# Performance work log

Hardware: AMD Instinct MI355X
Metric: run time of the kernel (lower is better)

The kernel has to match this reference:

```python
import jax, jax.numpy as jnp
import numpy as np

Nc, Nd, Ns = 8000, 6000, 6000          # circRNA / drug / disease node counts
F, H, O = 64, 4, 64                    # feature dim (fcir=fdrug=fdis), GAT heads, cnn out_channels
Ec, Ed, Es = 256000, 192000, 192000    # directed edge counts per graph
NEG_SLOPE = 0.2


def _gcn(x, src, dst, ew, W, b, N):
    # PyG GCNConv w/ edge_weight: add self loops (w=1), symmetric norm, x@W.T, scatter-add
    loop = jnp.arange(N, dtype=src.dtype)
    s = jnp.concatenate([src, loop])
    d = jnp.concatenate([dst, loop])
    w = jnp.concatenate([ew, jnp.ones((N,), x.dtype)])
    deg = jax.ops.segment_sum(w, d, num_segments=N)
    dinv = jnp.where(deg > 0, jax.lax.rsqrt(deg), 0.0)
    norm = dinv[s] * w * dinv[d]                        # [E+N]
    h = x @ W.T                                         # [N,F]
    return jax.ops.segment_sum(h[s] * norm[:, None], d, num_segments=N) + b


def _gat(x, src, dst, ew, W, a_src, a_dst, We, a_edge, b, N):
    # PyG GATConv(heads=H, concat=False, edge_dim=1); self loops with fill_value='mean'
    E = src.shape[0]
    ea = ew[:, None]                                    # [E,1]
    cnt = jax.ops.segment_sum(jnp.ones((E,), x.dtype), dst, num_segments=N)
    esum = jax.ops.segment_sum(ea, dst, num_segments=N)
    loop_attr = esum / jnp.maximum(cnt, 1.0)[:, None]   # per-dst mean edge attr
    loop = jnp.arange(N, dtype=src.dtype)
    s = jnp.concatenate([src, loop])
    d = jnp.concatenate([dst, loop])
    ea = jnp.concatenate([ea, loop_attr], axis=0)       # [E+N,1]
    h = (x @ W.T).reshape(N, H, F)
    al_s = jnp.einsum('nhf,hf->nh', h, a_src)
    al_d = jnp.einsum('nhf,hf->nh', h, a_dst)
    e = (ea @ We.T).reshape(-1, H, F)
    al_e = jnp.einsum('ehf,hf->eh', e, a_edge)
    alpha = al_s[s] + al_d[d] + al_e                    # [E+N,H]
    alpha = jnp.where(alpha >= 0, alpha, NEG_SLOPE * alpha)   # leaky_relu
    amax = jax.ops.segment_max(alpha, d, num_segments=N)
    ex = jnp.exp(alpha - amax[d])
    denom = jax.ops.segment_sum(ex, d, num_segments=N)
    coef = ex / denom[d]                                # segment softmax over incoming edges
    out = jax.ops.segment_sum(h[s] * coef[:, :, None], d, num_segments=N)  # [N,H,F]
    return out.mean(axis=1) + b                         # concat=False -> head mean


def _readout(x1, x2, W, b):
    # Conv1d(in=2, out=O, kernel=(F,1)) on [1,2,F,N] == full contraction over (layer, feature)
    X = jnp.stack([x1, x2], axis=0)                     # [2,N,F]
    return jnp.einsum('cnf,ocf->no', X, W) + b          # [N,O]


def _forward(fl, cir_edges, drug_edges, dis_edges):
    def branch(x, ei, ew, g1W, g1b, gaW, gas, gad, gaeW, gae, gab, g2W, g2b, N):
        src, dst = ei[0], ei[1]
        f1 = jax.nn.relu(_gcn(x, src, dst, ew, g1W, g1b, N))
        att = jax.nn.relu(_gat(f1, src, dst, ew, gaW, gas, gad, gaeW, gae, gab, N))
        f2 = jax.nn.relu(_gcn(att, src, dst, ew, g2W, g2b, N))
        return f1, f2

    cf1, cf2 = branch(fl['x_cir'], cir_edges, fl['cir_ew'], fl['gcn_cir1_W'], fl['gcn_cir1_b'],
                      fl['gat_cir_W'], fl['gat_cir_asrc'], fl['gat_cir_adst'], fl['gat_cir_eW'],
                      fl['gat_cir_aedge'], fl['gat_cir_b'], fl['gcn_cir2_W'], fl['gcn_cir2_b'], Nc)
    # NOTE: the source forward reuses the *_dis GCN/GAT layers for the drug branch (faithful)
    df1, df2 = branch(fl['x_drug'], drug_edges, fl['drug_ew'], fl['gcn_dis1_W'], fl['gcn_dis1_b'],
                      fl['gat_dis_W'], fl['gat_dis_asrc'], fl['gat_dis_adst'], fl['gat_dis_eW'],
                      fl['gat_dis_aedge'], fl['gat_dis_b'], fl['gcn_dis2_W'], fl['gcn_dis2_b'], Nd)
    sf1, sf2 = branch(fl['x_dis'], dis_edges, fl['dis_ew'], fl['gcn_dis1_W'], fl['gcn_dis1_b'],
                      fl['gat_dis_W'], fl['gat_dis_asrc'], fl['gat_dis_adst'], fl['gat_dis_eW'],
                      fl['gat_dis_aedge'], fl['gat_dis_b'], fl['gcn_dis2_W'], fl['gcn_dis2_b'], Ns)
    cir_fea = _readout(cf1, cf2, fl['cnn_cir_W'], fl['cnn_cir_b'])
    drug_fea = _readout(df1, df2, fl['cnn_dis_W'], fl['cnn_dis_b'])   # source uses cnn_dis for drug too
    dis_fea = _readout(sf1, sf2, fl['cnn_dis_W'], fl['cnn_dis_b'])
    return (cir_fea @ dis_fea.T, cir_fea @ drug_fea.T, drug_fea @ dis_fea.T,
            cir_fea, drug_fea, dis_fea)


_PARAM_SHAPES = [
    ('gcn_cir1_W', (F, F)), ('gcn_cir1_b', (F,)),
    ('gcn_cir2_W', (F, F)), ('gcn_cir2_b', (F,)),
    ('gcn_dis1_W', (F, F)), ('gcn_dis1_b', (F,)),
    ('gcn_dis2_W', (F, F)), ('gcn_dis2_b', (F,)),
    ('gat_cir_W', (H * F, F)), ('gat_cir_asrc', (H, F)), ('gat_cir_adst', (H, F)),
    ('gat_cir_eW', (H * F, 1)), ('gat_cir_aedge', (H, F)), ('gat_cir_b', (F,)),
    ('gat_dis_W', (H * F, F)), ('gat_dis_asrc', (H, F)), ('gat_dis_adst', (H, F)),
    ('gat_dis_eW', (H * F, 1)), ('gat_dis_aedge', (H, F)), ('gat_dis_b', (F,)),
    ('cnn_cir_W', (O, 2, F)), ('cnn_cir_b', (O,)),
    ('cnn_dis_W', (O, 2, F)), ('cnn_dis_b', (O,)),
]


def setup_inputs() -> dict:
    key = jax.random.key(0)
    ks = iter(jax.random.split(key, 64))
    inp = {}
    inp['x_cir'] = jax.random.normal(next(ks), (Nc, F), jnp.float32)
    inp['x_drug'] = jax.random.normal(next(ks), (Nd, F), jnp.float32)
    inp['x_dis'] = jax.random.normal(next(ks), (Ns, F), jnp.float32)
    inp['cir_edges'] = jax.random.randint(next(ks), (2, Ec), 0, Nc, dtype=jnp.int32)
    inp['cir_ew'] = jax.random.uniform(next(ks), (Ec,), jnp.float32)
    inp['drug_edges'] = jax.random.randint(next(ks), (2, Ed), 0, Nd, dtype=jnp.int32)
    inp['drug_ew'] = jax.random.uniform(next(ks), (Ed,), jnp.float32)
    inp['dis_edges'] = jax.random.randint(next(ks), (2, Es), 0, Ns, dtype=jnp.int32)
    inp['dis_ew'] = jax.random.uniform(next(ks), (Es,), jnp.float32)
    for name, shape in _PARAM_SHAPES:
        inp[name] = jax.random.normal(next(ks), shape, jnp.float32) * 0.1
    return inp


def reference(x_cir, x_drug, x_dis, cir_edges, cir_ew, drug_edges, drug_ew, dis_edges, dis_ew,
              gcn_cir1_W, gcn_cir1_b, gcn_cir2_W, gcn_cir2_b,
              gcn_dis1_W, gcn_dis1_b, gcn_dis2_W, gcn_dis2_b,
              gat_cir_W, gat_cir_asrc, gat_cir_adst, gat_cir_eW, gat_cir_aedge, gat_cir_b,
              gat_dis_W, gat_dis_asrc, gat_dis_adst, gat_dis_eW, gat_dis_aedge, gat_dis_b,
              cnn_cir_W, cnn_cir_b, cnn_dis_W, cnn_dis_b):
    fl = {k: v for k, v in locals().items() if k not in ('cir_edges', 'drug_edges', 'dis_edges')}
    return _forward(fl, cir_edges, drug_edges, dis_edges)
```

## Files before the change

kernel.cpp:

```cpp
#include <hip/hip_runtime.h>

#define NEG_SLOPE 0.2f

typedef __attribute__((ext_vector_type(8))) short bfrag;
typedef __attribute__((ext_vector_type(4))) float f32x4;

static __device__ __forceinline__ ushort f2bf(float x){
  uint u = __float_as_uint(x);
  uint r = (u + 0x7fff + ((u>>16)&1)) >> 16;
  return (ushort)r;
}
static __device__ __forceinline__ float bf2f(ushort h){
  return __uint_as_float(((uint)h)<<16);
}


struct G3 {
  const int* src[3]; const int* dst[3]; const float* ew[3];
  float* deg[3]; int* cnt[3]; int* pos[3];
  float* dinv[3]; float* lat[3]; int* rowp[3];
  int* esrc[3]; float* eww[3];
  int N[3]; int E[3];
};

struct MM3 {
  const float* A[3]; const float* B[3]; float* C[3]; const float* bias[3];
  ushort* H[3]; ushort* L[3];
  const float* gas[3]; const float* gad[3];
  float* als[3]; float* ald[3];
  int M[3]; int lda, ldb, N2;
};

struct AGG3 {
  const float* h[3]; const float* dinv[3]; const int* rowp[3];
  const int* esrc[3]; const float* eww[3]; const float* bias[3];
  float* out[3]; int N[3]; int ostride, ooff;
};

struct GAT3 {
  const float* hg[3]; const float* als[3]; const float* ald[3];
  const float* lat[3]; const float* ce[3]; const int* rowp[3];
  const int* esrc[3]; const float* eww[3]; const float* bias[3];
  float* out[3]; int N[3];
};

struct SC3 {
  const ushort* AH[3]; const ushort* AL[3];
  const ushort* BH[3]; const ushort* BL[3];
  float* C[3]; int M[3]; int N2;
};


__global__ void k_init_b(G3 g){
  int b = blockIdx.z;
  int i = blockIdx.x*blockDim.x + threadIdx.x;
  if (i < g.N[b]){ g.deg[b][i] = 1.0f; g.cnt[b][i] = 0; g.pos[b][i] = 0; }
}

__global__ void k_edge_stats_b(G3 g){
  int b = blockIdx.z;
  int e = blockIdx.x*blockDim.x + threadIdx.x;
  if (e < g.E[b]){
    int d = g.dst[b][e];
    atomicAdd(&g.deg[b][d], g.ew[b][e]);
    atomicAdd(&g.cnt[b][d], 1);
  }
}

__global__ void k_scan_b(G3 g, const float* gaeW_c, const float* gae_c, float* ce_c,
                         const float* gaeW_d, const float* gae_d, float* ce_d){
  int b = blockIdx.x;
  int tid = threadIdx.x;
  if (b < 2 && tid < 64){
    const float* W = b ? gaeW_d : gaeW_c;
    const float* Aa = b ? gae_d : gae_c;
    float* ceo = b ? ce_d : ce_c;
    #pragma unroll
    for (int hh=0; hh<4; hh++){
      float v = W[hh*64+tid] * Aa[hh*64+tid];
      #pragma unroll
      for (int off=32; off>0; off>>=1) v += __shfl_down(v,off);
      if (tid==0) ceo[hh] = v;
    }
  }
  int N = g.N[b];
  const float* deg = g.deg[b];
  const int* cnt = g.cnt[b];
  float* dinv = g.dinv[b];
  float* lat = g.lat[b];
  int* rowp = g.rowp[b];
  const int T = 1024, PER = 8;
  __shared__ int ssum[T];
  int base = tid*PER;
  int loc[PER]; int s = 0;
  #pragma unroll
  for (int u=0;u<PER;u++){
    int i = base+u;
    int c = (i<N)? cnt[i] : 0;
    loc[u] = s; s += c;
    if (i<N){
      float d = deg[i];
      dinv[i] = rsqrtf(d);
      lat[i] = (d - 1.0f) / fmaxf((float)c, 1.0f);
    }
  }
  ssum[tid] = s; __syncthreads();
  for (int off=1; off<T; off<<=1){
    int t = (tid>=off)? ssum[tid-off] : 0;
    __syncthreads();
    ssum[tid] += t;
    __syncthreads();
  }
  int excl = ssum[tid] - s;
  #pragma unroll
  for (int u=0;u<PER;u++){ int i=base+u; if (i<N) rowp[i] = excl + loc[u]; }
  if (tid == T-1) rowp[N] = ssum[T-1];
}

__global__ void k_scatter_b(G3 g){
  int b = blockIdx.z;
  int e = blockIdx.x*blockDim.x + threadIdx.x;
  if (e < g.E[b]){
    int d = g.dst[b][e];
    int p = g.rowp[b][d] + atomicAdd(&g.pos[b][d], 1);
    g.esrc[b][p] = g.src[b][e];
    g.eww[b][p] = g.ew[b][e];
  }
}


template<int K, bool BIAS, bool SPLIT, bool ALQ>
__global__ __launch_bounds__(256)
void k_mm_b(MM3 P){
  int br = blockIdx.z;
  int M = P.M[br];
  int bi = blockIdx.y*128;
  if (bi >= M) return;
  int N2 = P.N2;
  int bj = blockIdx.x*128;
  const float* __restrict__ A = P.A[br];
  const float* __restrict__ B = P.B[br];
  float* __restrict__ C = P.C[br];
  int lda = P.lda, ldb = P.ldb;

  __shared__ float As[128*36];
  __shared__ float Bs[32*132];
  int tid = threadIdx.x;
  int tx = tid & 15, ty = tid >> 4;
  float acc[8][8] = {};

  for (int kh = 0; kh < K; kh += 32){
    for (int t = tid; t < 1024; t += 256){
      int r = t >> 3, k4 = (t & 7) << 2;
      int gr = bi + r;
      float4 v = (gr < M) ? *(const float4*)(A + (size_t)gr*lda + kh + k4)
                          : make_float4(0.f,0.f,0.f,0.f);
      *(float4*)(As + r*36 + k4) = v;
    }
    for (int t = tid; t < 1024; t += 256){
      int r = t >> 3, k4 = (t & 7) << 2;
      int gr = bj + r;
      float4 v = (gr < N2) ? *(const float4*)(B + (size_t)gr*ldb + kh + k4)
                           : make_float4(0.f,0.f,0.f,0.f);
      Bs[(k4+0)*132 + r] = v.x;
      Bs[(k4+1)*132 + r] = v.y;
      Bs[(k4+2)*132 + r] = v.z;
      Bs[(k4+3)*132 + r] = v.w;
    }
    __syncthreads();
    #pragma unroll
    for (int k = 0; k < 32; k += 4){
      float4 a4[8];
      #pragma unroll
      for (int u=0; u<4; u++){
        a4[u]   = *(const float4*)(As + (ty*4+u)*36 + k);
        a4[u+4] = *(const float4*)(As + (64+ty*4+u)*36 + k);
      }
      #pragma unroll
      for (int i=0; i<4; i++){
        float4 bl = *(const float4*)(Bs + (k+i)*132 + tx*4);
        float4 bh = *(const float4*)(Bs + (k+i)*132 + 64 + tx*4);
        #pragma unroll
        for (int u=0; u<8; u++){
          float av = (i==0)?a4[u].x : (i==1)?a4[u].y : (i==2)?a4[u].z : a4[u].w;
          acc[u][0] += av*bl.x; acc[u][1] += av*bl.y;
          acc[u][2] += av*bl.z; acc[u][3] += av*bl.w;
          acc[u][4] += av*bh.x; acc[u][5] += av*bh.y;
          acc[u][6] += av*bh.z; acc[u][7] += av*bh.w;
        }
      }
    }
    __syncthreads();
  }

  #pragma unroll
  for (int u=0; u<8; u++){
    int gi = bi + ((u<4) ? (ty*4+u) : (64+ty*4+(u-4)));
    if (gi >= M) continue;
    #pragma unroll
    for (int half=0; half<2; half++){
      int gj = bj + ((half==0) ? tx*4 : 64+tx*4);
      int v0 = half*4;
      if (gj + 4 <= N2){
        float4 r4 = make_float4(acc[u][v0],acc[u][v0+1],acc[u][v0+2],acc[u][v0+3]);
        if (BIAS){
          const float* bb = P.bias[br];
          r4.x += bb[gj]; r4.y += bb[gj+1]; r4.z += bb[gj+2]; r4.w += bb[gj+3];
        }
        *(float4*)(C + (size_t)gi*N2 + gj) = r4;
        if (SPLIT){
          ushort hv[4], lv[4];
          float vv[4] = {r4.x, r4.y, r4.z, r4.w};
          #pragma unroll
          for (int v=0; v<4; v++){
            hv[v] = f2bf(vv[v]);
            lv[v] = f2bf(vv[v] - bf2f(hv[v]));
          }
          *(ushort4*)(P.H[br] + (size_t)gi*N2 + gj) = make_ushort4(hv[0],hv[1],hv[2],hv[3]);
          *(ushort4*)(P.L[br] + (size_t)gi*N2 + gj) = make_ushort4(lv[0],lv[1],lv[2],lv[3]);
        }
      } else {
        for (int v=0; v<4; v++) if (gj+v < N2){
          float r = acc[u][v0+v];
          if (BIAS) r += P.bias[br][gj+v];
          C[(size_t)gi*N2+gj+v] = r;
        }
      }
    }
  }

  if (ALQ){
    int h0 = bj >> 6;
    float ps[8][2], pd[8][2];
    #pragma unroll
    for (int u=0;u<8;u++){ ps[u][0]=0.f; ps[u][1]=0.f; pd[u][0]=0.f; pd[u][1]=0.f; }
    #pragma unroll
    for (int half=0; half<2; half++){
      #pragma unroll
      for (int v=0; v<4; v++){
        int cw = tx*4 + v;
        float gs = P.gas[br][(h0+half)*64 + cw];
        float gd = P.gad[br][(h0+half)*64 + cw];
        #pragma unroll
        for (int u=0;u<8;u++){
          ps[u][half] += acc[u][half*4+v]*gs;
          pd[u][half] += acc[u][half*4+v]*gd;
        }
      }
    }
    #pragma unroll
    for (int u=0;u<8;u++){
      #pragma unroll
      for (int hf=0; hf<2; hf++){
        float s = ps[u][hf], d = pd[u][hf];
        #pragma unroll
        for (int off=8; off>0; off>>=1){ s += __shfl_down(s,off); d += __shfl_down(d,off); }
        if (tx==0){
          int gi = bi + ((u<4) ? (ty*4+u) : (64+ty*4+(u-4)));
          if (gi < M){
            P.als[br][gi*4 + h0 + hf] = s;
            P.ald[br][gi*4 + h0 + hf] = d;
          }
        }
      }
    }
  }
}


__global__ void k_gcn_agg_b(AGG3 P){
  int b = blockIdx.z;
  int wid = (blockIdx.x*blockDim.x + threadIdx.x) >> 6;
  int f = threadIdx.x & 63;
  if (wid >= P.N[b]) return;
  const float* __restrict__ h = P.h[b];
  const float* __restrict__ dinv = P.dinv[b];
  const int* __restrict__ es = P.esrc[b];
  const float* __restrict__ ww = P.eww[b];
  float dn = dinv[wid];
  float acc = dn*dn*h[(size_t)wid*64 + f];
  int p0 = P.rowp[b][wid], p1 = P.rowp[b][wid+1];
  for (int p=p0; p<p1; p++){
    int s = es[p];
    float nrm = dinv[s]*ww[p]*dn;
    acc += nrm * h[(size_t)s*64 + f];
  }
  P.out[b][(size_t)wid*P.ostride + P.ooff + f] = fmaxf(acc + P.bias[b][f], 0.f);
}


__global__ void k_gat_agg_b(GAT3 P){
  int b = blockIdx.z;
  int wid = (blockIdx.x*blockDim.x + threadIdx.x) >> 6;
  int f = threadIdx.x & 63;
  if (wid >= P.N[b]) return;
  const float* __restrict__ hg = P.hg[b];
  const float* __restrict__ als = P.als[b];
  const int* __restrict__ es = P.esrc[b];
  const float* __restrict__ ww = P.eww[b];
  float4 cv = *(const float4*)P.ce[b];
  float c[4] = {cv.x, cv.y, cv.z, cv.w};
  float4 adv = *(const float4*)(P.ald[b] + (size_t)wid*4);
  float ad[4] = {adv.x, adv.y, adv.z, adv.w};
  float4 asv = *(const float4*)(als + (size_t)wid*4);
  float as_[4] = {asv.x, asv.y, asv.z, asv.w};
  float la = P.lat[b][wid];

  float m[4], l[4], acc[4];
  const float* hn = hg + (size_t)wid*256;
  #pragma unroll
  for (int hh=0; hh<4; hh++){
    float a = as_[hh] + ad[hh] + la*c[hh];
    a = (a >= 0.f) ? a : NEG_SLOPE*a;
    m[hh] = a; l[hh] = 1.f;
    acc[hh] = hn[hh*64 + f];
  }
  int p0 = P.rowp[b][wid], p1 = P.rowp[b][wid+1];
  for (int p=p0; p<p1; p++){
    int s = es[p];
    float w = ww[p];
    const float* hs = hg + (size_t)s*256;
    float4 asf = *(const float4*)(als + (size_t)s*4);
    float av[4] = {asf.x, asf.y, asf.z, asf.w};
    #pragma unroll
    for (int hh=0; hh<4; hh++){
      float a = av[hh] + ad[hh] + w*c[hh];
      a = (a >= 0.f) ? a : NEG_SLOPE*a;
      float mn = fmaxf(m[hh], a);
      float sc = __expf(m[hh] - mn);
      float fc = __expf(a - mn);
      acc[hh] = acc[hh]*sc + hs[hh*64+f]*fc;
      l[hh] = l[hh]*sc + fc;
      m[hh] = mn;
    }
  }
  float o = 0.25f*(acc[0]/l[0] + acc[1]/l[1] + acc[2]/l[2] + acc[3]/l[3]);
  P.out[b][(size_t)wid*64 + f] = fmaxf(o + P.bias[b][f], 0.f);
}


__global__ __launch_bounds__(256)
void k_score(SC3 P){
  int br = blockIdx.z;
  int M = P.M[br];
  int bi = blockIdx.y*128;
  if (bi >= M) return;
  int N = P.N2;
  int bj = blockIdx.x*128;
  const ushort* __restrict__ AH = P.AH[br];
  const ushort* __restrict__ ALo = P.AL[br];
  const ushort* __restrict__ BH = P.BH[br];
  const ushort* __restrict__ BLo = P.BL[br];
  float* __restrict__ C = P.C[br];

  int wv = threadIdx.x >> 6;
  int lane = threadIdx.x & 63;
  int la = lane & 15, lk = lane >> 4;
  int r0 = bi + (wv>>1)*64;
  int c0 = bj + (wv&1)*64;

  bfrag ah[4][2], al[4][2];
  #pragma unroll
  for (int mi=0; mi<4; mi++){
    int r = r0 + mi*16 + la; if (r > M-1) r = M-1;
    size_t base = (size_t)r*64 + lk*8;
    ah[mi][0] = *(const bfrag*)(AH + base);
    ah[mi][1] = *(const bfrag*)(AH + base + 32);
    al[mi][0] = *(const bfrag*)(ALo + base);
    al[mi][1] = *(const bfrag*)(ALo + base + 32);
  }

  f32x4 acc[4][4];
  #pragma unroll
  for (int mi=0; mi<4; mi++)
    #pragma unroll
    for (int ni=0; ni<4; ni++)
      acc[mi][ni] = (f32x4){0.f,0.f,0.f,0.f};

  #pragma unroll
  for (int ni=0; ni<4; ni++){
    int cc = c0 + ni*16 + la; if (cc > N-1) cc = N-1;
    size_t base = (size_t)cc*64 + lk*8;
    bfrag bh0 = *(const bfrag*)(BH + base);
    bfrag bh1 = *(const bfrag*)(BH + base + 32);
    bfrag bl0 = *(const bfrag*)(BLo + base);
    bfrag bl1 = *(const bfrag*)(BLo + base + 32);
    #pragma unroll
    for (int mi=0; mi<4; mi++){
      f32x4 a = acc[mi][ni];
      a = __builtin_amdgcn_mfma_f32_16x16x32_bf16(ah[mi][0], bh0, a, 0, 0, 0);
      a = __builtin_amdgcn_mfma_f32_16x16x32_bf16(ah[mi][1], bh1, a, 0, 0, 0);
      a = __builtin_amdgcn_mfma_f32_16x16x32_bf16(ah[mi][0], bl0, a, 0, 0, 0);
      a = __builtin_amdgcn_mfma_f32_16x16x32_bf16(ah[mi][1], bl1, a, 0, 0, 0);
      a = __builtin_amdgcn_mfma_f32_16x16x32_bf16(al[mi][0], bh0, a, 0, 0, 0);
      a = __builtin_amdgcn_mfma_f32_16x16x32_bf16(al[mi][1], bh1, a, 0, 0, 0);
      acc[mi][ni] = a;
    }
  }

  #pragma unroll
  for (int mi=0; mi<4; mi++){
    int rb = r0 + mi*16 + lk*4;
    #pragma unroll
    for (int ni=0; ni<4; ni++){
      int col = c0 + ni*16 + la;
      if (col >= N) continue;
      #pragma unroll
      for (int rg=0; rg<4; rg++){
        int r = rb + rg;
        if (r < M) C[(size_t)r*N + col] = acc[mi][ni][rg];
      }
    }
  }
}


extern "C" void kernel_launch(void* const* d_in, const int* in_sizes, int n_in,
                              void* d_out, int out_size, void* d_ws, size_t ws_size,
                              hipStream_t stream){
  const float* x_cir  = (const float*)d_in[0];
  const float* x_drug = (const float*)d_in[1];
  const float* x_dis  = (const float*)d_in[2];
  const int*   cir_edges  = (const int*)d_in[3];
  const float* cir_ew     = (const float*)d_in[4];
  const int*   drug_edges = (const int*)d_in[5];
  const float* drug_ew    = (const float*)d_in[6];
  const int*   dis_edges  = (const int*)d_in[7];
  const float* dis_ew     = (const float*)d_in[8];
  const float* gcn_cir1_W = (const float*)d_in[9];
  const float* gcn_cir1_b = (const float*)d_in[10];
  const float* gcn_cir2_W = (const float*)d_in[11];
  const float* gcn_cir2_b = (const float*)d_in[12];
  const float* gcn_dis1_W = (const float*)d_in[13];
  const float* gcn_dis1_b = (const float*)d_in[14];
  const float* gcn_dis2_W = (const float*)d_in[15];
  const float* gcn_dis2_b = (const float*)d_in[16];
  const float* gat_cir_W    = (const float*)d_in[17];
  const float* gat_cir_asrc = (const float*)d_in[18];
  const float* gat_cir_adst = (const float*)d_in[19];
  const float* gat_cir_eW   = (const float*)d_in[20];
  const float* gat_cir_aedge= (const float*)d_in[21];
  const float* gat_cir_b    = (const float*)d_in[22];
  const float* gat_dis_W    = (const float*)d_in[23];
  const float* gat_dis_asrc = (const float*)d_in[24];
  const float* gat_dis_adst = (const float*)d_in[25];
  const float* gat_dis_eW   = (const float*)d_in[26];
  const float* gat_dis_aedge= (const float*)d_in[27];
  const float* gat_dis_b    = (const float*)d_in[28];
  const float* cnn_cir_W = (const float*)d_in[29];
  const float* cnn_cir_b = (const float*)d_in[30];
  const float* cnn_dis_W = (const float*)d_in[31];
  const float* cnn_dis_b = (const float*)d_in[32];
  float* out = (float*)d_out;

  const int Nb[3] = {8000, 6000, 6000};
  const int Eb[3] = {256000, 192000, 192000};

  char* wp = (char*)d_ws;
  auto alloc = [&](size_t bytes)->void*{
    void* p = wp; wp += (bytes + 255) & ~(size_t)255; return p;
  };

  float* fea[3] = { out + 132000000ULL, out + 132512000ULL, out + 132896000ULL };

  float* ce_c = (float*)alloc(64);
  float* ce_d = (float*)alloc(64);

  G3 g;
  const int* edges[3] = {cir_edges, drug_edges, dis_edges};
  const float* ews[3] = {cir_ew, drug_ew, dis_ew};
  float *hbuf[3], *f12[3], *att[3], *als[3], *ald[3];
  ushort *feaH[3], *feaL[3];
  for (int b=0; b<3; b++){
    g.src[b] = edges[b];
    g.dst[b] = edges[b] + Eb[b];
    g.ew[b]  = ews[b];
    g.N[b] = Nb[b]; g.E[b] = Eb[b];
    g.deg[b]  = (float*)alloc((size_t)Nb[b]*4);
    g.dinv[b] = (float*)alloc((size_t)Nb[b]*4);
    g.lat[b]  = (float*)alloc((size_t)Nb[b]*4);
    g.cnt[b]  = (int*)alloc((size_t)Nb[b]*4);
    g.pos[b]  = (int*)alloc((size_t)Nb[b]*4);
    g.rowp[b] = (int*)alloc((size_t)(Nb[b]+1)*4);
    g.esrc[b] = (int*)alloc((size_t)Eb[b]*4);
    g.eww[b]  = (float*)alloc((size_t)Eb[b]*4);
    als[b]  = (float*)alloc((size_t)Nb[b]*4*4);
    ald[b]  = (float*)alloc((size_t)Nb[b]*4*4);
    hbuf[b] = (float*)alloc((size_t)Nb[b]*256*4);
    f12[b]  = (float*)alloc((size_t)Nb[b]*128*4);
    att[b]  = (float*)alloc((size_t)Nb[b]*64*4);
    feaH[b] = (ushort*)alloc((size_t)Nb[b]*64*2);
    feaL[b] = (ushort*)alloc((size_t)Nb[b]*64*2);
  }

  const float* xin[3]  = {x_cir, x_drug, x_dis};
  const float* g1W[3]  = {gcn_cir1_W, gcn_dis1_W, gcn_dis1_W};
  const float* g1b[3]  = {gcn_cir1_b, gcn_dis1_b, gcn_dis1_b};
  const float* g2W[3]  = {gcn_cir2_W, gcn_dis2_W, gcn_dis2_W};
  const float* g2b[3]  = {gcn_cir2_b, gcn_dis2_b, gcn_dis2_b};
  const float* gaW[3]  = {gat_cir_W, gat_dis_W, gat_dis_W};
  const float* gasP[3] = {gat_cir_asrc, gat_dis_asrc, gat_dis_asrc};
  const float* gadP[3] = {gat_cir_adst, gat_dis_adst, gat_dis_adst};
  const float* gab[3]  = {gat_cir_b, gat_dis_b, gat_dis_b};
  const float* cep[3]  = {ce_c, ce_d, ce_d};
  const float* cW[3]   = {cnn_cir_W, cnn_dis_W, cnn_dis_W};
  const float* cb[3]   = {cnn_cir_b, cnn_dis_b, cnn_dis_b};

  k_init_b<<<dim3(32,1,3),256,0,stream>>>(g);
  k_edge_stats_b<<<dim3(1000,1,3),256,0,stream>>>(g);
  k_scan_b<<<3,1024,0,stream>>>(g, gat_cir_eW, gat_cir_aedge, ce_c,
                                   gat_dis_eW, gat_dis_aedge, ce_d);
  k_scatter_b<<<dim3(1000,1,3),256,0,stream>>>(g);

  auto mkmm = [&](MM3& m, const float* const* Ap, const float* const* Bp,
                  float* const* Cp, const float* const* bp, int lda, int ldb, int N2){
    for (int b=0;b<3;b++){
      m.A[b]=Ap[b]; m.B[b]=Bp[b]; m.C[b]=Cp[b]; m.bias[b]= bp? bp[b] : nullptr;
      m.H[b]=nullptr; m.L[b]=nullptr;
      m.gas[b]=nullptr; m.gad[b]=nullptr; m.als[b]=nullptr; m.ald[b]=nullptr;
      m.M[b]=Nb[b];
    }
    m.lda=lda; m.ldb=ldb; m.N2=N2;
  };

  MM3 m1; mkmm(m1, xin, g1W, hbuf, nullptr, 64, 64, 64);
  k_mm_b<64,false,false,false><<<dim3(1,63,3),256,0,stream>>>(m1);

  AGG3 a1;
  for (int b=0;b<3;b++){ a1.h[b]=hbuf[b]; a1.dinv[b]=g.dinv[b]; a1.rowp[b]=g.rowp[b];
    a1.esrc[b]=g.esrc[b]; a1.eww[b]=g.eww[b]; a1.bias[b]=g1b[b]; a1.out[b]=f12[b]; a1.N[b]=Nb[b]; }
  a1.ostride=128; a1.ooff=0;
  k_gcn_agg_b<<<dim3(2000,1,3),256,0,stream>>>(a1);

  {
    const float* Ap[3] = {f12[0], f12[1], f12[2]};
    MM3 m2; mkmm(m2, Ap, gaW, hbuf, nullptr, 128, 64, 256);
    for (int b=0;b<3;b++){ m2.gas[b]=gasP[b]; m2.gad[b]=gadP[b]; m2.als[b]=als[b]; m2.ald[b]=ald[b]; }
    k_mm_b<64,false,false,true><<<dim3(2,63,3),256,0,stream>>>(m2);
  }

  GAT3 gt;
  for (int b=0;b<3;b++){ gt.hg[b]=hbuf[b]; gt.als[b]=als[b]; gt.ald[b]=ald[b]; gt.lat[b]=g.lat[b];
    gt.ce[b]=cep[b]; gt.rowp[b]=g.rowp[b]; gt.esrc[b]=g.esrc[b]; gt.eww[b]=g.eww[b];
    gt.bias[b]=gab[b]; gt.out[b]=att[b]; gt.N[b]=Nb[b]; }
  k_gat_agg_b<<<dim3(2000,1,3),256,0,stream>>>(gt);

  {
    const float* Ap[3] = {att[0], att[1], att[2]};
    MM3 m3; mkmm(m3, Ap, g2W, hbuf, nullptr, 64, 64, 64);
    k_mm_b<64,false,false,false><<<dim3(1,63,3),256,0,stream>>>(m3);
  }

  AGG3 a2 = a1;
  for (int b=0;b<3;b++){ a2.bias[b]=g2b[b]; }
  a2.ooff=64;
  k_gcn_agg_b<<<dim3(2000,1,3),256,0,stream>>>(a2);

  {
    const float* Ap[3] = {f12[0], f12[1], f12[2]};
    MM3 m4; mkmm(m4, Ap, cW, fea, cb, 128, 128, 64);
    for (int b=0;b<3;b++){ m4.H[b]=feaH[b]; m4.L[b]=feaL[b]; }
    k_mm_b<128,true,true,false><<<dim3(1,63,3),256,0,stream>>>(m4);
  }

  SC3 sc;
  sc.AH[0]=feaH[0]; sc.AL[0]=feaL[0]; sc.BH[0]=feaH[2]; sc.BL[0]=feaL[2];
  sc.C[0]=out;               sc.M[0]=8000;
  sc.AH[1]=feaH[0]; sc.AL[1]=feaL[0]; sc.BH[1]=feaH[1]; sc.BL[1]=feaL[1];
  sc.C[1]=out + 48000000ULL; sc.M[1]=8000;
  sc.AH[2]=feaH[1]; sc.AL[2]=feaL[1]; sc.BH[2]=feaH[2]; sc.BL[2]=feaL[2];
  sc.C[2]=out + 96000000ULL; sc.M[2]=6000;
  sc.N2=6000;
  k_score<<<dim3(47,63,3),256,0,stream>>>(sc);
}
```

Before: 1.053 ms.

## Pack CSR edges, prefold GCN norm, two-pass GAT with lane-parallel attention

The scatter now writes one packed int4 per edge holding the source, the weight and dinv[src]*weight, so the GCN aggregation does a single load and one fma per edge. The init kernel is folded into the first matmul launch as an extra column of blocks. The GAT aggregation becomes two passes: a max pass, then a sum pass, each computing attention for 16 edges by 4 heads across lanes and broadcasting through readlane. This replaces the serial per-edge online softmax with exp rescaling. The cost is a second walk over each edge list and a wider 16-byte edge record.

After: 1.029 ms. 2.2% less time.

```diff
diff --git a/kernel.cpp b/kernel.cpp
--- a/kernel.cpp
+++ b/kernel.cpp
@@ -13,13 +13,16 @@
 static __device__ __forceinline__ float bf2f(ushort h){
   return __uint_as_float(((uint)h)<<16);
 }
+static __device__ __forceinline__ float rdlane(float v, int l){
+  return __int_as_float(__builtin_amdgcn_readlane(__float_as_int(v), l));
+}
 
 
 struct G3 {
   const int* src[3]; const int* dst[3]; const float* ew[3];
   float* deg[3]; int* cnt[3]; int* pos[3];
   float* dinv[3]; float* lat[3]; int* rowp[3];
-  int* esrc[3]; float* eww[3];
+  int4* ep[3];
   int N[3]; int E[3];
 };
 
@@ -33,14 +36,14 @@
 
 struct AGG3 {
   const float* h[3]; const float* dinv[3]; const int* rowp[3];
-  const int* esrc[3]; const float* eww[3]; const float* bias[3];
+  const int4* ep[3]; const float* bias[3];
   float* out[3]; int N[3]; int ostride, ooff;
 };
 
 struct GAT3 {
   const float* hg[3]; const float* als[3]; const float* ald[3];
   const float* lat[3]; const float* ce[3]; const int* rowp[3];
-  const int* esrc[3]; const float* eww[3]; const float* bias[3];
+  const int4* ep[3]; const float* bias[3];
   float* out[3]; int N[3];
 };
 
@@ -50,12 +53,6 @@
   float* C[3]; int M[3]; int N2;
 };
 
-
-__global__ void k_init_b(G3 g){
-  int b = blockIdx.z;
-  int i = blockIdx.x*blockDim.x + threadIdx.x;
-  if (i < g.N[b]){ g.deg[b][i] = 1.0f; g.cnt[b][i] = 0; g.pos[b][i] = 0; }
-}
 
 __global__ void k_edge_stats_b(G3 g){
   int b = blockIdx.z;
@@ -122,16 +119,24 @@
   int e = blockIdx.x*blockDim.x + threadIdx.x;
   if (e < g.E[b]){
     int d = g.dst[b][e];
+    int s = g.src[b][e];
+    float w = g.ew[b][e];
+    float dw = g.dinv[b][s] * w;
     int p = g.rowp[b][d] + atomicAdd(&g.pos[b][d], 1);
-    g.esrc[b][p] = g.src[b][e];
-    g.eww[b][p] = g.ew[b][e];
-  }
-}
-
-
-template<int K, bool BIAS, bool SPLIT, bool ALQ>
+    g.ep[b][p] = make_int4(s, __float_as_int(w), __float_as_int(dw), 0);
+  }
+}
+
+
+template<int K, bool BIAS, bool SPLIT, bool ALQ, bool INIT>
 __global__ __launch_bounds__(256)
-void k_mm_b(MM3 P){
+void k_mm_b(MM3 P, G3 g){
+  if (INIT && blockIdx.x == gridDim.x-1){
+    int b = blockIdx.z;
+    int i = blockIdx.y*256 + threadIdx.x;
+    if (i < g.N[b]){ g.deg[b][i] = 1.0f; g.cnt[b][i] = 0; g.pos[b][i] = 0; }
+    return;
+  }
   int br = blockIdx.z;
   int M = P.M[br];
   int bi = blockIdx.y*128;
@@ -274,68 +279,98 @@
   int f = threadIdx.x & 63;
   if (wid >= P.N[b]) return;
   const float* __restrict__ h = P.h[b];
-  const float* __restrict__ dinv = P.dinv[b];
-  const int* __restrict__ es = P.esrc[b];
-  const float* __restrict__ ww = P.eww[b];
-  float dn = dinv[wid];
-  float acc = dn*dn*h[(size_t)wid*64 + f];
+  const int4* __restrict__ ep = P.ep[b];
+  float dn = P.dinv[b][wid];
+  float acc = dn*h[(size_t)wid*64 + f];
   int p0 = P.rowp[b][wid], p1 = P.rowp[b][wid+1];
   for (int p=p0; p<p1; p++){
-    int s = es[p];
-    float nrm = dinv[s]*ww[p]*dn;
-    acc += nrm * h[(size_t)s*64 + f];
-  }
-  P.out[b][(size_t)wid*P.ostride + P.ooff + f] = fmaxf(acc + P.bias[b][f], 0.f);
+    int4 pr = ep[p];
+    acc = fmaf(__int_as_float(pr.z), h[(size_t)pr.x*64 + f], acc);
+  }
+  P.out[b][(size_t)wid*P.ostride + P.ooff + f] = fmaxf(fmaf(dn, acc, P.bias[b][f]), 0.f);
 }
 
 
 __global__ void k_gat_agg_b(GAT3 P){
   int b = blockIdx.z;
   int wid = (blockIdx.x*blockDim.x + threadIdx.x) >> 6;
-  int f = threadIdx.x & 63;
+  int lane = threadIdx.x & 63;
   if (wid >= P.N[b]) return;
   const float* __restrict__ hg = P.hg[b];
   const float* __restrict__ als = P.als[b];
-  const int* __restrict__ es = P.esrc[b];
-  const float* __restrict__ ww = P.eww[b];
+  const int4* __restrict__ ep = P.ep[b];
+  int h = lane & 3;
+  int el = lane >> 2;
+  int f = lane;
+
   float4 cv = *(const float4*)P.ce[b];
-  float c[4] = {cv.x, cv.y, cv.z, cv.w};
   float4 adv = *(const float4*)(P.ald[b] + (size_t)wid*4);
-  float ad[4] = {adv.x, adv.y, adv.z, adv.w};
   float4 asv = *(const float4*)(als + (size_t)wid*4);
-  float as_[4] = {asv.x, asv.y, asv.z, asv.w};
+  float c_l  = (h==0)?cv.x :(h==1)?cv.y :(h==2)?cv.z :cv.w;
+  float ad_l = (h==0)?adv.x:(h==1)?adv.y:(h==2)?adv.z:adv.w;
+  float as_l = (h==0)?asv.x:(h==1)?asv.y:(h==2)?asv.z:asv.w;
   float la = P.lat[b][wid];
 
-  float m[4], l[4], acc[4];
+  float a_self = as_l + ad_l + la*c_l;
+  a_self = (a_self >= 0.f) ? a_self : NEG_SLOPE*a_self;
+  float m = a_self;
+
+  int p0 = P.rowp[b][wid], p1 = P.rowp[b][wid+1];
+
+  for (int c0=p0; c0<p1; c0+=16){
+    int idx = c0 + el;
+    float a = -1e30f;
+    if (idx < p1){
+      int4 pr = ep[idx];
+      float w = __int_as_float(pr.y);
+      a = als[pr.x*4 + h] + ad_l + w*c_l;
+      a = (a >= 0.f) ? a : NEG_SLOPE*a;
+    }
+    #pragma unroll
+    for (int off=4; off<64; off<<=1) a = fmaxf(a, __shfl_xor(a, off));
+    m = fmaxf(m, a);
+  }
+
+  float ex_self = __expf(a_self - m);
+  float l = ex_self;
   const float* hn = hg + (size_t)wid*256;
-  #pragma unroll
-  for (int hh=0; hh<4; hh++){
-    float a = as_[hh] + ad[hh] + la*c[hh];
-    a = (a >= 0.f) ? a : NEG_SLOPE*a;
-    m[hh] = a; l[hh] = 1.f;
-    acc[hh] = hn[hh*64 + f];
-  }
-  int p0 = P.rowp[b][wid], p1 = P.rowp[b][wid+1];
-  for (int p=p0; p<p1; p++){
-    int s = es[p];
-    float w = ww[p];
-    const float* hs = hg + (size_t)s*256;
-    float4 asf = *(const float4*)(als + (size_t)s*4);
-    float av[4] = {asf.x, asf.y, asf.z, asf.w};
-    #pragma unroll
-    for (int hh=0; hh<4; hh++){
-      float a = av[hh] + ad[hh] + w*c[hh];
+  float acc0 = rdlane(ex_self,0) * hn[f];
+  float acc1 = rdlane(ex_self,1) * hn[64+f];
+  float acc2 = rdlane(ex_self,2) * hn[128+f];
+  float acc3 = rdlane(ex_self,3) * hn[192+f];
+
+  for (int c0=p0; c0<p1; c0+=16){
+    int idx = c0 + el;
+    float ex = 0.f;
+    int s_lane = 0;
+    if (idx < p1){
+      int4 pr = ep[idx];
+      s_lane = pr.x;
+      float w = __int_as_float(pr.y);
+      float a = als[s_lane*4 + h] + ad_l + w*c_l;
       a = (a >= 0.f) ? a : NEG_SLOPE*a;
-      float mn = fmaxf(m[hh], a);
-      float sc = __expf(m[hh] - mn);
-      float fc = __expf(a - mn);
-      acc[hh] = acc[hh]*sc + hs[hh*64+f]*fc;
-      l[hh] = l[hh]*sc + fc;
-      m[hh] = mn;
-    }
-  }
-  float o = 0.25f*(acc[0]/l[0] + acc[1]/l[1] + acc[2]/l[2] + acc[3]/l[3]);
-  P.out[b][(size_t)wid*64 + f] = fmaxf(o + P.bias[b][f], 0.f);
+      ex = __expf(a - m);
+    }
+    float ls = ex;
+    #pragma unroll
+    for (int off=4; off<64; off<<=1) ls += __shfl_xor(ls, off);
+    l += ls;
+    int cnt = p1 - c0; if (cnt > 16) cnt = 16;
+    for (int e=0; e<cnt; e++){
+      int s = __builtin_amdgcn_readlane(s_lane, e*4);
+      const float* hs = hg + (size_t)s*256 + f;
+      float x0 = rdlane(ex, e*4+0);
+      float x1 = rdlane(ex, e*4+1);
+      float x2 = rdlane(ex, e*4+2);
+      float x3 = rdlane(ex, e*4+3);
+      acc0 = fmaf(x0, hs[0],   acc0);
+      acc1 = fmaf(x1, hs[64],  acc1);
+      acc2 = fmaf(x2, hs[128], acc2);
+      acc3 = fmaf(x3, hs[192], acc3);
+    }
+  }
+  float o = acc0/rdlane(l,0) + acc1/rdlane(l,1) + acc2/rdlane(l,2) + acc3/rdlane(l,3);
+  P.out[b][(size_t)wid*64 + f] = fmaxf(0.25f*o + P.bias[b][f], 0.f);
 }
 
 
@@ -482,8 +517,7 @@
     g.cnt[b]  = (int*)alloc((size_t)Nb[b]*4);
     g.pos[b]  = (int*)alloc((size_t)Nb[b]*4);
     g.rowp[b] = (int*)alloc((size_t)(Nb[b]+1)*4);
-    g.esrc[b] = (int*)alloc((size_t)Eb[b]*4);
-    g.eww[b]  = (float*)alloc((size_t)Eb[b]*4);
+    g.ep[b]   = (int4*)alloc((size_t)Eb[b]*16);
     als[b]  = (float*)alloc((size_t)Nb[b]*4*4);
     ald[b]  = (float*)alloc((size_t)Nb[b]*4*4);
     hbuf[b] = (float*)alloc((size_t)Nb[b]*256*4);
@@ -506,12 +540,6 @@
   const float* cW[3]   = {cnn_cir_W, cnn_dis_W, cnn_dis_W};
   const float* cb[3]   = {cnn_cir_b, cnn_dis_b, cnn_dis_b};
 
-  k_init_b<<<dim3(32,1,3),256,0,stream>>>(g);
-  k_edge_stats_b<<<dim3(1000,1,3),256,0,stream>>>(g);
-  k_scan_b<<<3,1024,0,stream>>>(g, gat_cir_eW, gat_cir_aedge, ce_c,
-                                   gat_dis_eW, gat_dis_aedge, ce_d);
-  k_scatter_b<<<dim3(1000,1,3),256,0,stream>>>(g);
-
   auto mkmm = [&](MM3& m, const float* const* Ap, const float* const* Bp,
                   float* const* Cp, const float* const* bp, int lda, int ldb, int N2){
     for (int b=0;b<3;b++){
@@ -524,11 +552,16 @@
   };
 
   MM3 m1; mkmm(m1, xin, g1W, hbuf, nullptr, 64, 64, 64);
-  k_mm_b<64,false,false,false><<<dim3(1,63,3),256,0,stream>>>(m1);
+  k_mm_b<64,false,false,false,true><<<dim3(2,63,3),256,0,stream>>>(m1, g);
+
+  k_edge_stats_b<<<dim3(1000,1,3),256,0,stream>>>(g);
+  k_scan_b<<<3,1024,0,stream>>>(g, gat_cir_eW, gat_cir_aedge, ce_c,
+                                   gat_dis_eW, gat_dis_aedge, ce_d);
+  k_scatter_b<<<dim3(1000,1,3),256,0,stream>>>(g);
 
   AGG3 a1;
   for (int b=0;b<3;b++){ a1.h[b]=hbuf[b]; a1.dinv[b]=g.dinv[b]; a1.rowp[b]=g.rowp[b];
-    a1.esrc[b]=g.esrc[b]; a1.eww[b]=g.eww[b]; a1.bias[b]=g1b[b]; a1.out[b]=f12[b]; a1.N[b]=Nb[b]; }
+    a1.ep[b]=g.ep[b]; a1.bias[b]=g1b[b]; a1.out[b]=f12[b]; a1.N[b]=Nb[b]; }
   a1.ostride=128; a1.ooff=0;
   k_gcn_agg_b<<<dim3(2000,1,3),256,0,stream>>>(a1);
 
@@ -536,19 +569,19 @@
     const float* Ap[3] = {f12[0], f12[1], f12[2]};
     MM3 m2; mkmm(m2, Ap, gaW, hbuf, nullptr, 128, 64, 256);
     for (int b=0;b<3;b++){ m2.gas[b]=gasP[b]; m2.gad[b]=gadP[b]; m2.als[b]=als[b]; m2.ald[b]=ald[b]; }
-    k_mm_b<64,false,false,true><<<dim3(2,63,3),256,0,stream>>>(m2);
+    k_mm_b<64,false,false,true,false><<<dim3(2,63,3),256,0,stream>>>(m2, g);
   }
 
   GAT3 gt;
   for (int b=0;b<3;b++){ gt.hg[b]=hbuf[b]; gt.als[b]=als[b]; gt.ald[b]=ald[b]; gt.lat[b]=g.lat[b];
-    gt.ce[b]=cep[b]; gt.rowp[b]=g.rowp[b]; gt.esrc[b]=g.esrc[b]; gt.eww[b]=g.eww[b];
+    gt.ce[b]=cep[b]; gt.rowp[b]=g.rowp[b]; gt.ep[b]=g.ep[b];
     gt.bias[b]=gab[b]; gt.out[b]=att[b]; gt.N[b]=Nb[b]; }
   k_gat_agg_b<<<dim3(2000,1,3),256,0,stream>>>(gt);
 
   {
     const float* Ap[3] = {att[0], att[1], att[2]};
     MM3 m3; mkmm(m3, Ap, g2W, hbuf, nullptr, 64, 64, 64);
-    k_mm_b<64,false,false,false><<<dim3(1,63,3),256,0,stream>>>(m3);
+    k_mm_b<64,false,false,false,false><<<dim3(1,63,3),256,0,stream>>>(m3, g);
   }
 
   AGG3 a2 = a1;
@@ -560,7 +593,7 @@
     const float* Ap[3] = {f12[0], f12[1], f12[2]};
     MM3 m4; mkmm(m4, Ap, cW, fea, cb, 128, 128, 64);
     for (int b=0;b<3;b++){ m4.H[b]=feaH[b]; m4.L[b]=feaL[b]; }
-    k_mm_b<128,true,true,false><<<dim3(1,63,3),256,0,stream>>>(m4);
+    k_mm_b<128,true,true,false,false><<<dim3(1,63,3),256,0,stream>>>(m4, g);
   }
 
   SC3 sc;
```
